# Performance work log

Hardware: AMD Instinct MI355X
Metric: run time of the kernel (lower is better)

## Reference

```python
import jax, jax.numpy as jnp
import numpy as np

D_MODEL = 1024
N_HEADS = 16
HEAD_DIM = D_MODEL // N_HEADS
MAX_POS = 4096
ROPE_BASE = 10000.0
NEG_INF = -1e30


def _rope_cache(max_pos, head_dim, base):
    inv_freq = 1.0 / (base ** (np.arange(0, head_dim, 2, dtype=np.float32) / head_dim))
    t = np.arange(max_pos, dtype=np.float32)[:, None] * inv_freq[None, :]  # [P, D/2]
    cos = np.repeat(np.cos(t), 2, axis=-1)  # [P, D] (repeat_interleave)
    sin = np.repeat(np.sin(t), 2, axis=-1)
    return jnp.asarray(cos), jnp.asarray(sin)

COS_CACHE, SIN_CACHE = _rope_cache(MAX_POS, HEAD_DIM, ROPE_BASE)


def _rotate_half(x):
    # interleaved pairs: (x0,x1,x2,x3,...) -> (-x1,x0,-x3,x2,...)
    x1 = x[..., ::2]
    x2 = x[..., 1::2]
    return jnp.stack((-x2, x1), axis=-1).reshape(x.shape)


def setup_inputs() -> dict:
    key = jax.random.key(0)
    k0, k1, k2 = jax.random.split(key, 3)
    B, S = 4, 1024
    hidden_states = jax.random.normal(k0, (B, S, D_MODEL), dtype=jnp.float32)
    positions = jnp.arange(S, dtype=jnp.int64 if jax.config.jax_enable_x64 else jnp.int32)
    causal_mask = jnp.triu(jnp.ones((S, S), dtype=bool), k=1)  # True above diagonal -> masked
    # learned params (torch nn.Linear weight layout: [out, in], y = x @ W.T)
    Wqkv = jax.random.normal(k1, (3 * D_MODEL, D_MODEL), dtype=jnp.float32) * (D_MODEL ** -0.5)
    Wout = jax.random.normal(k2, (D_MODEL, D_MODEL), dtype=jnp.float32) * (D_MODEL ** -0.5)
    return {"hidden_states": hidden_states, "positions": positions,
            "causal_mask": causal_mask, "Wqkv": Wqkv, "Wout": Wout}


def reference(hidden_states, positions, causal_mask, Wqkv, Wout):
    B, S, D = hidden_states.shape
    qkv = hidden_states @ Wqkv.T                                   # [B,S,3D]
    qkv = qkv.reshape(B, S, 3, N_HEADS, HEAD_DIM)
    qkv = jnp.transpose(qkv, (2, 0, 3, 1, 4))                      # [3,B,H,S,Dh]
    q, k, v = qkv[0], qkv[1], qkv[2]
    # RoPE
    pos = jnp.clip(positions, 0, MAX_POS - 1)
    if pos.ndim == 1:
        pos = pos[None, :]
    cos = COS_CACHE[pos][:, None, :, :].astype(q.dtype)            # [B,1,S,Dh]
    sin = SIN_CACHE[pos][:, None, :, :].astype(q.dtype)
    q = q * cos + _rotate_half(q) * sin
    k = k * cos + _rotate_half(k) * sin
    # SDPA with causal bias (F.scaled_dot_product_attention default scaling)
    scale = HEAD_DIM ** -0.5
    scores = jnp.einsum('bhqd,bhkd->bhqk', q, k) * scale           # [B,H,S,S]
    scores = jnp.where(causal_mask[None, None, :, :], NEG_INF, scores)
    probs = jax.nn.softmax(scores, axis=-1)
    attn = jnp.einsum('bhqk,bhkd->bhqd', probs, v)                 # [B,H,S,Dh]
    attn = jnp.transpose(attn, (0, 2, 1, 3)).reshape(B, S, D)
    return attn @ Wout.T
```

## Files before the change

### kernel.cpp

```cpp
#include <hip/hip_runtime.h>

typedef __attribute__((ext_vector_type(8))) short short8;
typedef __attribute__((ext_vector_type(4))) float f32x4;

#define MFMA(a, b, c) __builtin_amdgcn_mfma_f32_16x16x32_bf16((a), (b), (c), 0, 0, 0)

#define S_LEN 1024
#define DM 1024
#define NHEADS 16
#define HD 64
#define NBH 64
#define MAXPOS 4096

__device__ __forceinline__ ushort f2bf(float f) {
    unsigned u = __builtin_bit_cast(unsigned, f);
    u += 0x7fffu + ((u >> 16) & 1u);
    return (ushort)(u >> 16);
}
__device__ __forceinline__ float bf2f(ushort h) {
    return __builtin_bit_cast(float, (unsigned)h << 16);
}

__device__ __forceinline__ void gload16(const ushort* g, ushort* l) {
    __builtin_amdgcn_global_load_lds(
        (const __attribute__((address_space(1))) unsigned int*)g,
        (__attribute__((address_space(3))) unsigned int*)l, 16, 0, 0);
}

__global__ __launch_bounds__(256) void k_build_tab(float* __restrict__ tab) {
    int id = blockIdx.x * 256 + threadIdx.x;
    int p = id >> 5, i = id & 31;
    float inv = powf(10000.f, -(float)(2 * i) / 64.f);
    float t = (float)p * inv;
    float s, c;
    sincosf(t, &s, &c);
    tab[2 * id] = c;
    tab[2 * id + 1] = s;
}

__global__ __launch_bounds__(256) void k_cvt(const float4* __restrict__ in,
                                             ushort4* __restrict__ outp, int n4) {
    int id = blockIdx.x * 256 + threadIdx.x;
    if (id >= n4) return;
    float4 v = in[id];
    ushort4 o;
    o.x = f2bf(v.x); o.y = f2bf(v.y); o.z = f2bf(v.z); o.w = f2bf(v.w);
    outp[id] = o;
}

template <int MODE>
__global__ __launch_bounds__(256, 2) void k_gemm(
    const ushort* __restrict__ A, const ushort* __restrict__ BT,
    float* __restrict__ Cf,
    const int* __restrict__ pos, const float* __restrict__ tab,
    ushort* __restrict__ Qh, ushort* __restrict__ Kh, ushort* __restrict__ Vt,
    int M, int N, int K, int nbx) {
    __shared__ __align__(16) ushort SH[4 * 128 * 64];
    const int tid = threadIdx.x;
    const int lane = tid & 63, wave = tid >> 6;
    const int wr = wave >> 1, wc = wave & 1;
    const int l15 = lane & 15, lhi = lane >> 4;
    const int cpx = gridDim.x >> 3;
    const int wg = (blockIdx.x & 7) * cpx + (blockIdx.x >> 3);
    const int by = wg / nbx, bx = wg - by * nbx;
    const int m0 = by << 7, n0 = bx << 7;
    const int lr = tid >> 3;
    const int lc = (tid & 7) << 3;

    f32x4 acc[4][4];
#pragma unroll
    for (int i = 0; i < 4; ++i)
#pragma unroll
        for (int j = 0; j < 4; ++j) acc[i][j] = 0;

#define STAGE(buf, kb)                                                          \
    do {                                                                        \
        ushort* ab = SH + (buf) * 16384;                                        \
        _Pragma("unroll") for (int i = 0; i < 4; ++i)                           \
            gload16(&A[(size_t)(m0 + i * 32 + lr) * K + (kb) + lc],             \
                    ab + (i * 32 + lr) * 64 + lc);                              \
        _Pragma("unroll") for (int i = 0; i < 4; ++i)                           \
            gload16(&BT[(size_t)(n0 + i * 32 + lr) * K + (kb) + lc],            \
                    ab + 8192 + (i * 32 + lr) * 64 + lc);                       \
    } while (0)

    STAGE(0, 0);
    __syncthreads();
    int cur = 0;
    const int nk = K >> 6;
    for (int t = 0; t < nk; ++t) {
        if (t + 1 < nk) STAGE(cur ^ 1, (t + 1) << 6);
        const ushort* Ab = SH + cur * 16384;
        const ushort* Bb = Ab + 8192;
        __builtin_amdgcn_s_setprio(1);
#pragma unroll
        for (int kk = 0; kk < 2; ++kk) {
            short8 a[4], b[4];
#pragma unroll
            for (int fm = 0; fm < 4; ++fm)
                a[fm] = *(const short8*)&Ab[(wr * 64 + fm * 16 + l15) * 64 + kk * 32 + lhi * 8];
#pragma unroll
            for (int fn = 0; fn < 4; ++fn)
                b[fn] = *(const short8*)&Bb[(wc * 64 + fn * 16 + l15) * 64 + kk * 32 + lhi * 8];
#pragma unroll
            for (int fm = 0; fm < 4; ++fm)
#pragma unroll
                for (int fn = 0; fn < 4; ++fn)
                    acc[fm][fn] = MFMA(a[fm], b[fn], acc[fm][fn]);
        }
        __builtin_amdgcn_s_setprio(0);
        __syncthreads();
        cur ^= 1;
    }
#undef STAGE

    if (MODE == 0) {
#pragma unroll
        for (int fm = 0; fm < 4; ++fm)
#pragma unroll
            for (int fn = 0; fn < 4; ++fn)
#pragma unroll
                for (int i = 0; i < 4; ++i) {
                    int row = m0 + wr * 64 + fm * 16 + lhi * 4 + i;
                    int col = n0 + wc * 64 + fn * 16 + l15;
                    Cf[(size_t)row * N + col] = acc[fm][fn][i];
                }
    } else {
        const int sec = n0 >> 10;
        if (sec < 2) {
            ushort* dstb = sec == 0 ? Qh : Kh;
            const float qs = sec == 0 ? 0.125f : 1.0f;
#pragma unroll
            for (int fm = 0; fm < 4; ++fm)
#pragma unroll
                for (int i = 0; i < 4; ++i) {
                    const int row = m0 + wr * 64 + fm * 16 + lhi * 4 + i;
                    const int b = row >> 10, s = row & 1023;
                    int p = pos[s];
                    p = p < 0 ? 0 : (p > MAXPOS - 1 ? MAXPOS - 1 : p);
#pragma unroll
                    for (int fn = 0; fn < 4; ++fn) {
                        const int col = n0 + wc * 64 + fn * 16 + l15;
                        const int cw = col & 1023;
                        const int h = cw >> 6, d = cw & 63;
                        const float c  = tab[((size_t)p * 32 + (d >> 1)) * 2];
                        const float sn = tab[((size_t)p * 32 + (d >> 1)) * 2 + 1];
                        const float v = acc[fm][fn][i];
                        const float pr = __shfl_xor(v, 1);
                        const float o = (d & 1) ? (v * c + pr * sn) : (v * c - pr * sn);
                        dstb[((size_t)((b * 16 + h) * 1024 + s)) * 64 + d] = f2bf(o * qs);
                    }
                }
        } else {
            ushort (*T)[132] = (ushort(*)[132]) & SH[0];
#pragma unroll
            for (int fm = 0; fm < 4; ++fm)
#pragma unroll
                for (int fn = 0; fn < 4; ++fn)
#pragma unroll
                    for (int i = 0; i < 4; ++i)
                        T[wr * 64 + fm * 16 + lhi * 4 + i][wc * 64 + fn * 16 + l15] =
                            f2bf(acc[fm][fn][i]);
            __syncthreads();
            const int b = m0 >> 10, s0 = m0 & 1023;
            const int dd = tid & 127, scg = tid >> 7;
            const int hv = ((n0 & 1023) >> 6) + (dd >> 6);
            const int d = dd & 63;
            ushort* dst = Vt + ((size_t)(b * 16 + hv) * 64 + d) * S_LEN + s0;
#pragma unroll
            for (int j = 0; j < 8; ++j) {
                const int ch = scg * 8 + j;
                __align__(16) ushort tmp[8];
#pragma unroll
                for (int e = 0; e < 8; ++e) tmp[e] = T[ch * 8 + e][dd];
                *(uint4*)&dst[ch * 8] = *(uint4*)tmp;
            }
        }
    }
}

__global__ __launch_bounds__(256, 3) void k_attn(const ushort* __restrict__ Qh,
                                                 const ushort* __restrict__ Kh,
                                                 const ushort* __restrict__ Vt,
                                                 ushort* __restrict__ attnB) {
    __shared__ __align__(16) ushort Ks[2][64][64];
    __shared__ __align__(16) ushort Vs[2][64][64];
    __shared__ __align__(16) ushort P[4][16][72];
    const int bh = blockIdx.x;
    const int g  = 15 - blockIdx.y;
    const int tid = threadIdx.x;
    const int wave = tid >> 6, lane = tid & 63;
    const int l15 = lane & 15, lhi = lane >> 4;
    const int b = bh >> 4, h = bh & 15;
    const ushort* Qp = Qh + (size_t)bh * S_LEN * 64;
    const ushort* Kp = Kh + (size_t)bh * S_LEN * 64;
    const ushort* Vp = Vt + (size_t)bh * 64 * S_LEN;
    const int qb = (g << 6) + (wave << 4);
    const int qrowb = qb + lhi * 4;

    const int U0 = tid, U1 = tid + 256;
    const int r0 = U0 >> 3, o0 = ((U0 & 7) ^ (r0 & 7)) << 3;
    const int r1 = U1 >> 3, o1 = ((U1 & 7) ^ (r1 & 7)) << 3;
    ushort* KsF = &Ks[0][0][0];
    ushort* VsF = &Vs[0][0][0];

    short8 aQ0 = *(const short8*)&Qp[(size_t)(qb + l15) * 64 + lhi * 8];
    short8 aQ1 = *(const short8*)&Qp[(size_t)(qb + l15) * 64 + 32 + lhi * 8];

    short8 ones;
#pragma unroll
    for (int j = 0; j < 8; ++j) ones[j] = (short)0x3F80;

    f32x4 O0{}, O1{}, O2{}, O3{}, ssum{};

    gload16(&Kp[(size_t)r0 * 64 + o0], KsF + U0 * 8);
    gload16(&Kp[(size_t)r1 * 64 + o1], KsF + U1 * 8);
    gload16(&Vp[(size_t)r0 * S_LEN + o0], VsF + U0 * 8);
    gload16(&Vp[(size_t)r1 * S_LEN + o1], VsF + U1 * 8);
    __syncthreads();

#define LDSK(s, kk) (*(const short8*)(KsF + (cur << 12) + ((((s) << 4) + l15) << 6) + \
                                      ((((kk) * 4 + lhi) ^ (l15 & 7)) << 3)))
#define LDSV(n, kk) (*(const short8*)(VsF + (cur << 12) + ((((n) << 4) + l15) << 6) + \
                                      ((((kk) * 4 + lhi) ^ (l15 & 7)) << 3)))

    int cur = 0;
    for (int kb = 0; kb <= g; ++kb) {
        const int k0 = kb << 6;
        if (kb < g) {
            const int kn = k0 + 64;
            const int bo = (cur ^ 1) << 12;
            gload16(&Kp[(size_t)(kn + r0) * 64 + o0], KsF + bo + U0 * 8);
            gload16(&Kp[(size_t)(kn + r1) * 64 + o1], KsF + bo + U1 * 8);
            gload16(&Vp[(size_t)r0 * S_LEN + kn + o0], VsF + bo + U0 * 8);
            gload16(&Vp[(size_t)r1 * S_LEN + kn + o1], VsF + bo + U1 * 8);
        }

        __builtin_amdgcn_s_setprio(1);
        f32x4 s0{}, s1{}, s2{}, s3{};
        s0 = MFMA(aQ0, LDSK(0, 0), s0); s0 = MFMA(aQ1, LDSK(0, 1), s0);
        s1 = MFMA(aQ0, LDSK(1, 0), s1); s1 = MFMA(aQ1, LDSK(1, 1), s1);
        s2 = MFMA(aQ0, LDSK(2, 0), s2); s2 = MFMA(aQ1, LDSK(2, 1), s2);
        s3 = MFMA(aQ0, LDSK(3, 0), s3); s3 = MFMA(aQ1, LDSK(3, 1), s3);
        __builtin_amdgcn_s_setprio(0);

        if (kb == g) {
#define EXPSTM(SV, SUB)                                                        \
    _Pragma("unroll") for (int i = 0; i < 4; ++i) {                            \
        float v = SV[i];                                                       \
        if (k0 + (SUB) * 16 + l15 > qrowb + i) v = -1e30f;                     \
        P[wave][lhi * 4 + i][(SUB) * 16 + l15] = f2bf(__expf(v - 8.f));        \
    }
            EXPSTM(s0, 0) EXPSTM(s1, 1) EXPSTM(s2, 2) EXPSTM(s3, 3)
#undef EXPSTM
        } else {
#define EXPST(SV, SUB)                                                         \
    _Pragma("unroll") for (int i = 0; i < 4; ++i) {                            \
        P[wave][lhi * 4 + i][(SUB) * 16 + l15] = f2bf(__expf(SV[i] - 8.f));    \
    }
            EXPST(s0, 0) EXPST(s1, 1) EXPST(s2, 2) EXPST(s3, 3)
#undef EXPST
        }

        short8 aP0 = *(const short8*)&P[wave][l15][lhi * 8];
        short8 aP1 = *(const short8*)&P[wave][l15][32 + lhi * 8];
        __builtin_amdgcn_s_setprio(1);
        ssum = MFMA(aP0, ones, ssum); ssum = MFMA(aP1, ones, ssum);
        O0 = MFMA(aP0, LDSV(0, 0), O0); O0 = MFMA(aP1, LDSV(0, 1), O0);
        O1 = MFMA(aP0, LDSV(1, 0), O1); O1 = MFMA(aP1, LDSV(1, 1), O1);
        O2 = MFMA(aP0, LDSV(2, 0), O2); O2 = MFMA(aP1, LDSV(2, 1), O2);
        O3 = MFMA(aP0, LDSV(3, 0), O3); O3 = MFMA(aP1, LDSV(3, 1), O3);
        __builtin_amdgcn_s_setprio(0);

        __syncthreads();
        cur ^= 1;
    }
#undef LDSK
#undef LDSV

    f32x4 inv;
#pragma unroll
    for (int i = 0; i < 4; ++i) inv[i] = 1.f / ssum[i];
#define WOUT(OV, N)                                                            \
    _Pragma("unroll") for (int i = 0; i < 4; ++i) {                            \
        int row = qb + lhi * 4 + i;                                            \
        attnB[((size_t)(b * S_LEN + row)) * DM + h * 64 + (N) * 16 + l15] =    \
            f2bf(OV[i] * inv[i]);                                              \
    }
    WOUT(O0, 0) WOUT(O1, 1) WOUT(O2, 2) WOUT(O3, 3)
#undef WOUT
}

extern "C" void kernel_launch(void* const* d_in, const int* in_sizes, int n_in,
                              void* d_out, int out_size, void* d_ws, size_t ws_size,
                              hipStream_t stream) {
    (void)in_sizes; (void)n_in; (void)out_size; (void)ws_size;
    const float* hs   = (const float*)d_in[0];
    const int*   pos  = (const int*)d_in[1];
    const float* Wqkv = (const float*)d_in[3];
    const float* Wout = (const float*)d_in[4];
    float* out = (float*)d_out;

    char* ws = (char*)d_ws;
    size_t off = 0;
    ushort* hsB   = (ushort*)(ws + off); off += (size_t)4096 * 1024 * 2;
    ushort* WqkvB = (ushort*)(ws + off); off += (size_t)3072 * 1024 * 2;
    ushort* WoutB = (ushort*)(ws + off); off += (size_t)1024 * 1024 * 2;
    ushort* Qh    = (ushort*)(ws + off); off += (size_t)NBH * 1024 * 64 * 2;
    ushort* Kh    = (ushort*)(ws + off); off += (size_t)NBH * 1024 * 64 * 2;
    ushort* Vt    = (ushort*)(ws + off); off += (size_t)NBH * 64 * 1024 * 2;
    ushort* attnB = (ushort*)(ws + off); off += (size_t)4096 * 1024 * 2;
    float*  tab   = (float*)(ws + off);  off += (size_t)4096 * 32 * 2 * 4;

    k_build_tab<<<512, 256, 0, stream>>>(tab);
    k_cvt<<<4096, 256, 0, stream>>>((const float4*)hs,   (ushort4*)hsB,   1048576);
    k_cvt<<<3072, 256, 0, stream>>>((const float4*)Wqkv, (ushort4*)WqkvB,  786432);
    k_cvt<<<1024, 256, 0, stream>>>((const float4*)Wout, (ushort4*)WoutB,  262144);

    k_gemm<1><<<768, 256, 0, stream>>>(hsB, WqkvB, nullptr, pos, tab,
                                       Qh, Kh, Vt, 4096, 3072, 1024, 24);

    k_attn<<<dim3(64, 16), 256, 0, stream>>>(Qh, Kh, Vt, attnB);

    k_gemm<0><<<256, 256, 0, stream>>>(attnB, WoutB, out, nullptr, nullptr,
                                       nullptr, nullptr, nullptr, 4096, 1024, 1024, 8);
}
```

Baseline: 110.5 us.

## Triple-buffer GEMM K-loop with swizzled LDS and XCD-aware tile mapping

Restructures the bf16 GEMM main loop from a double-buffered 64-wide K step into a triple-buffered 32-wide K step. It uses explicit vmcnt waits and a single barrier per iteration, so global-to-LDS loads run two stages ahead. LDS tiles get an XOR swizzle on the column to avoid bank conflicts, and shared memory shrinks enough to allow three blocks per CU. Block-to-tile mapping is changed so each XCD covers a contiguous 2D region, to improve L2 reuse. The risks are higher register pressure from the occupancy bound and mapping assumptions about grid divisibility.

```diff
diff --git a/kernel.cpp b/kernel.cpp
--- a/kernel.cpp
+++ b/kernel.cpp
@@ -49,23 +49,27 @@
 }
 
 template <int MODE>
-__global__ __launch_bounds__(256, 2) void k_gemm(
+__global__ __launch_bounds__(256, 3) void k_gemm(
     const ushort* __restrict__ A, const ushort* __restrict__ BT,
     float* __restrict__ Cf,
     const int* __restrict__ pos, const float* __restrict__ tab,
     ushort* __restrict__ Qh, ushort* __restrict__ Kh, ushort* __restrict__ Vt,
     int M, int N, int K, int nbx) {
-    __shared__ __align__(16) ushort SH[4 * 128 * 64];
+    __shared__ __align__(16) ushort SH[3 * 8192];
     const int tid = threadIdx.x;
     const int lane = tid & 63, wave = tid >> 6;
     const int wr = wave >> 1, wc = wave & 1;
     const int l15 = lane & 15, lhi = lane >> 4;
-    const int cpx = gridDim.x >> 3;
-    const int wg = (blockIdx.x & 7) * cpx + (blockIdx.x >> 3);
-    const int by = wg / nbx, bx = wg - by * nbx;
+    const int nby = gridDim.x / nbx;
+    const int xcd = blockIdx.x & 7, idx = blockIdx.x >> 3;
+    const int Creg = nbx >> 1, Rreg = nby >> 2;
+    const int by = (xcd >> 1) * Rreg + idx / Creg;
+    const int bx = (xcd & 1) * Creg + idx % Creg;
     const int m0 = by << 7, n0 = bx << 7;
-    const int lr = tid >> 3;
-    const int lc = (tid & 7) << 3;
+
+    const int srow = tid >> 2;
+    const int scol = (((tid >> 2) & 3) ^ ((tid >> 4) & 3) ^ (tid & 3)) << 3;
+    const int fcol = ((lhi ^ ((l15 & 3) ^ ((l15 >> 2) & 3)))) << 3;
 
     f32x4 acc[4][4];
 #pragma unroll
@@ -73,46 +77,57 @@
 #pragma unroll
         for (int j = 0; j < 4; ++j) acc[i][j] = 0;
 
-#define STAGE(buf, kb)                                                          \
+#define STAGE(bs, kb)                                                           \
     do {                                                                        \
-        ushort* ab = SH + (buf) * 16384;                                        \
-        _Pragma("unroll") for (int i = 0; i < 4; ++i)                           \
-            gload16(&A[(size_t)(m0 + i * 32 + lr) * K + (kb) + lc],             \
-                    ab + (i * 32 + lr) * 64 + lc);                              \
-        _Pragma("unroll") for (int i = 0; i < 4; ++i)                           \
-            gload16(&BT[(size_t)(n0 + i * 32 + lr) * K + (kb) + lc],            \
-                    ab + 8192 + (i * 32 + lr) * 64 + lc);                       \
+        ushort* bb = SH + (bs) * 8192;                                          \
+        gload16(&A[(size_t)(m0 + srow) * K + (kb) + scol], bb + tid * 8);       \
+        gload16(&A[(size_t)(m0 + 64 + srow) * K + (kb) + scol],                 \
+                bb + 2048 + tid * 8);                                           \
+        gload16(&BT[(size_t)(n0 + srow) * K + (kb) + scol],                     \
+                bb + 4096 + tid * 8);                                           \
+        gload16(&BT[(size_t)(n0 + 64 + srow) * K + (kb) + scol],                \
+                bb + 6144 + tid * 8);                                           \
     } while (0)
 
+    const int nk = K >> 5;
     STAGE(0, 0);
+    STAGE(1, 32);
+    int bi = 0;
+    for (int t = 0; t < nk; ++t) {
+        if (t + 1 < nk) {
+            asm volatile("s_waitcnt vmcnt(4)" ::: "memory");
+        } else {
+            asm volatile("s_waitcnt vmcnt(0)" ::: "memory");
+        }
+        __builtin_amdgcn_s_barrier();
+        __builtin_amdgcn_sched_barrier(0);
+        if (t + 2 < nk) {
+            int bs = bi + 2;
+            if (bs >= 3) bs -= 3;
+            STAGE(bs, (t + 2) << 5);
+        }
+        const ushort* bufA = SH + bi * 8192;
+        const ushort* bufB = bufA + 4096;
+        short8 a[4], b[4];
+#pragma unroll
+        for (int fm = 0; fm < 4; ++fm)
+            a[fm] = *(const short8*)&bufA[(wr * 64 + fm * 16 + l15) * 32 + fcol];
+#pragma unroll
+        for (int fn = 0; fn < 4; ++fn)
+            b[fn] = *(const short8*)&bufB[(wc * 64 + fn * 16 + l15) * 32 + fcol];
+        asm volatile("s_waitcnt lgkmcnt(0)" ::: "memory");
+        __builtin_amdgcn_sched_barrier(0);
+        __builtin_amdgcn_s_setprio(1);
+#pragma unroll
+        for (int fm = 0; fm < 4; ++fm)
+#pragma unroll
+            for (int fn = 0; fn < 4; ++fn)
+                acc[fm][fn] = MFMA(a[fm], b[fn], acc[fm][fn]);
+        __builtin_amdgcn_s_setprio(0);
+        bi = (bi == 2) ? 0 : bi + 1;
+    }
+#undef STAGE
     __syncthreads();
-    int cur = 0;
-    const int nk = K >> 6;
-    for (int t = 0; t < nk; ++t) {
-        if (t + 1 < nk) STAGE(cur ^ 1, (t + 1) << 6);
-        const ushort* Ab = SH + cur * 16384;
-        const ushort* Bb = Ab + 8192;
-        __builtin_amdgcn_s_setprio(1);
-#pragma unroll
-        for (int kk = 0; kk < 2; ++kk) {
-            short8 a[4], b[4];
-#pragma unroll
-            for (int fm = 0; fm < 4; ++fm)
-                a[fm] = *(const short8*)&Ab[(wr * 64 + fm * 16 + l15) * 64 + kk * 32 + lhi * 8];
-#pragma unroll
-            for (int fn = 0; fn < 4; ++fn)
-                b[fn] = *(const short8*)&Bb[(wc * 64 + fn * 16 + l15) * 64 + kk * 32 + lhi * 8];
-#pragma unroll
-            for (int fm = 0; fm < 4; ++fm)
-#pragma unroll
-                for (int fn = 0; fn < 4; ++fn)
-                    acc[fm][fn] = MFMA(a[fm], b[fn], acc[fm][fn]);
-        }
-        __builtin_amdgcn_s_setprio(0);
-        __syncthreads();
-        cur ^= 1;
-    }
-#undef STAGE
 
     if (MODE == 0) {
 #pragma unroll
```

After: 98.87 us. 1.12x faster.
